# Kernel tuning notes

Measured on AMD Instinct MI355X. Metric: run time of the kernel, lower is better.

Reference implementation:

```python
import jax, jax.numpy as jnp
import numpy as np

NUM_HEADS = 4
NUM_GROUPS = 32
EPS = 1e-6


def group_norm(x, gamma, beta):
    # x: [b, c, h, w]
    b, c, h, w = x.shape
    xg = x.reshape(b, NUM_GROUPS, c // NUM_GROUPS, h, w)
    mu = xg.mean(axis=(2, 3, 4), keepdims=True)
    var = xg.var(axis=(2, 3, 4), keepdims=True)
    xn = ((xg - mu) * jax.lax.rsqrt(var + EPS)).reshape(b, c, h, w)
    return xn * gamma[None, :, None, None] + beta[None, :, None, None]


def conv1x1(x, W, b):
    # 1x1 conv == per-pixel channel matmul. W: [out_c, in_c], b: [out_c]
    return jnp.einsum('bchw,oc->bohw', x, W) + b[None, :, None, None]


def setup_inputs() -> dict:
    key = jax.random.key(0)
    ks = jax.random.split(key, 8)
    c = 256
    b, h, w = 1, 64, 64
    s = 1.0 / np.sqrt(c)
    return {
        'x_kv': jax.random.normal(ks[0], (b, c, h, w), dtype=jnp.float32),
        'gn_gamma': jnp.ones((c,), dtype=jnp.float32),
        'gn_beta': jnp.zeros((c,), dtype=jnp.float32),
        'Wq': jax.random.normal(ks[1], (c, c), dtype=jnp.float32) * s,
        'bq': jnp.zeros((c,), dtype=jnp.float32),
        'Wk': jax.random.normal(ks[2], (c, c), dtype=jnp.float32) * s,
        'bk': jnp.zeros((c,), dtype=jnp.float32),
        'Wv': jax.random.normal(ks[3], (c, c), dtype=jnp.float32) * s,
        'bv': jnp.zeros((c,), dtype=jnp.float32),
        'Wp': jax.random.normal(ks[4], (c, c), dtype=jnp.float32) * s,
        'bp': jnp.zeros((c,), dtype=jnp.float32),
    }


def reference(x_kv, gn_gamma, gn_beta, Wq, bq, Wk, bk, Wv, bv, Wp, bp):
    b, c, h, w = x_kv.shape
    hd = c // NUM_HEADS
    n = h * w

    h_norm = group_norm(x_kv, gn_gamma, gn_beta)  # self-attn: same norm for q,k,v

    q = conv1x1(h_norm, Wq, bq).reshape(b, NUM_HEADS, hd, n).transpose(0, 1, 3, 2)  # [b,H,n,hd]
    k = conv1x1(h_norm, Wk, bk).reshape(b, NUM_HEADS, hd, n)                        # [b,H,hd,n]
    v = conv1x1(h_norm, Wv, bv).reshape(b, NUM_HEADS, hd, n).transpose(0, 1, 3, 2)  # [b,H,n,hd]

    scores = jnp.einsum('bhnd,bhdm->bhnm', q, k) * (hd ** -0.5)  # [b,H,n,n]
    attn = jax.nn.softmax(scores, axis=-1)
    out = jnp.einsum('bhnm,bhmd->bhnd', attn, v)  # [b,H,n,hd]

    # Faithful to torch: permute(0,2,1,3).contiguous().view(b,c,h,w)
    out = out.transpose(0, 2, 1, 3).reshape(b, c, h, w)
    return x_kv + conv1x1(out, Wp, bp)
```

## Files before the change

### kernel.cpp

```cpp
#include <hip/hip_runtime.h>
#include <hip/hip_bf16.h>

#define NPIX 4096
#define CCH  256
#define HD   64
#define GSIZE 32768

typedef __bf16 bf16x8 __attribute__((ext_vector_type(8)));
typedef __bf16 bf16x4 __attribute__((ext_vector_type(4)));
typedef float  f32x4  __attribute__((ext_vector_type(4)));

#define XPITCH 264


__global__ __launch_bounds__(256) void stats_wconv(
    const float* __restrict__ X,
    const float* __restrict__ Wq, const float* __restrict__ Wk,
    const float* __restrict__ Wv, const float* __restrict__ Wp,
    float* __restrict__ psum, float* __restrict__ pssq, __bf16* __restrict__ Wb)
{
    const int bid = blockIdx.x, t = threadIdx.x;
    if (bid < 256) {
        const float* base = X + bid * 4096;
        float sum = 0.f, ssq = 0.f;
        #pragma unroll
        for (int k = 0; k < 4; ++k) {
            float4 v = *(const float4*)(base + t * 4 + k * 1024);
            sum += v.x + v.y + v.z + v.w;
            ssq += v.x * v.x + v.y * v.y + v.z * v.z + v.w * v.w;
        }
        #pragma unroll
        for (int off = 1; off < 64; off <<= 1) {
            sum += __shfl_xor(sum, off);
            ssq += __shfl_xor(ssq, off);
        }
        __shared__ float red[2][4];
        const int wv = t >> 6;
        if ((t & 63) == 0) { red[0][wv] = sum; red[1][wv] = ssq; }
        __syncthreads();
        if (t == 0) {
            psum[bid] = red[0][0] + red[0][1] + red[0][2] + red[0][3];
            pssq[bid] = red[1][0] + red[1][1] + red[1][2] + red[1][3];
        }
    } else {
        const int j0 = (bid - 256) * 4096 + t * 16;
        const int m  = j0 >> 16;
        const float* W = (m == 0) ? Wq : (m == 1) ? Wk : (m == 2) ? Wv : Wp;
        const float sc = (m == 0) ? 0.125f : 1.f;
        const int off = j0 & 65535;
        #pragma unroll
        for (int k = 0; k < 4; ++k) {
            float4 v = *(const float4*)(W + off + k * 4);
            bf16x4 o;
            o[0] = (__bf16)(v.x * sc); o[1] = (__bf16)(v.y * sc);
            o[2] = (__bf16)(v.z * sc); o[3] = (__bf16)(v.w * sc);
            *(bf16x4*)(Wb + m * 65536 + off + k * 4) = o;
        }
    }
}

__global__ __launch_bounds__(256) void gn_qkv(
    const float* __restrict__ X, const float* __restrict__ gamma,
    const float* __restrict__ beta,
    const float* __restrict__ psum, const float* __restrict__ pssq,
    const __bf16* __restrict__ Wb,
    const float* __restrict__ bq, const float* __restrict__ bk,
    const float* __restrict__ bv,
    __bf16* __restrict__ Qb, __bf16* __restrict__ Kb, __bf16* __restrict__ Vb)
{
    __shared__ __bf16 tile[64 * XPITCH];
    __shared__ float al[256], bl[256];

    const int t = threadIdx.x, lane = t & 63, wave = t >> 6;
    const int l16 = lane & 15, quad = lane >> 4;
    const int p0 = blockIdx.x * 64;
    const int z = blockIdx.y >> 1, och = blockIdx.y & 1;

    {
        const int g = t >> 3;
        float s = 0.f, q = 0.f;
        #pragma unroll
        for (int j = 0; j < 8; ++j) { s += psum[g * 8 + j]; q += pssq[g * 8 + j]; }
        const float mu  = s * (1.f / GSIZE);
        const float var = q * (1.f / GSIZE) - mu * mu;
        const float a = gamma[t] * rsqrtf(var + 1e-6f);
        al[t] = a;
        bl[t] = beta[t] - mu * a;
    }
    __syncthreads();

    #pragma unroll 4
    for (int i = 0; i < 16; ++i) {
        const int c4 = wave * 64 + i * 4;
        f32x4 a4 = *(const f32x4*)(al + c4);
        f32x4 b4 = *(const f32x4*)(bl + c4);
        bf16x4 pk;
        pk[0] = (__bf16)(X[(c4 + 0) * NPIX + p0 + lane] * a4[0] + b4[0]);
        pk[1] = (__bf16)(X[(c4 + 1) * NPIX + p0 + lane] * a4[1] + b4[1]);
        pk[2] = (__bf16)(X[(c4 + 2) * NPIX + p0 + lane] * a4[2] + b4[2]);
        pk[3] = (__bf16)(X[(c4 + 3) * NPIX + p0 + lane] * a4[3] + b4[3]);
        *(bf16x4*)(tile + lane * XPITCH + c4) = pk;
    }
    __syncthreads();

    const int pw = wave * 16;
    bf16x8 xf[8];
    #pragma unroll
    for (int kc = 0; kc < 8; ++kc)
        xf[kc] = *(const bf16x8*)(tile + (pw + l16) * XPITCH + kc * 32 + quad * 8);

    const __bf16* Wz = Wb + z * 65536;
    const float* bias = (z == 0) ? bq : (z == 1) ? bk : bv;

    if (z < 2) {
        const float qs = (z == 0) ? 0.125f : 1.f;
        __bf16* dst = (z == 0) ? Qb : Kb;
        #pragma unroll
        for (int grp = 0; grp < 2; ++grp) {
            f32x4 acc[4] = {};
            #pragma unroll
            for (int kc = 0; kc < 8; ++kc) {
                #pragma unroll
                for (int u = 0; u < 4; ++u) {
                    bf16x8 wf = *(const bf16x8*)(Wz + (och * 128 + (grp * 4 + u) * 16 + l16) * CCH + kc * 32 + quad * 8);
                    acc[u] = __builtin_amdgcn_mfma_f32_16x16x32_bf16(wf, xf[kc], acc[u], 0, 0, 0);
                }
            }
            #pragma unroll
            for (int u = 0; u < 4; ++u) {
                const int ot = och * 8 + grp * 4 + u;
                f32x4 bz = *(const f32x4*)(bias + och * 128 + (grp * 4 + u) * 16 + quad * 4);
                bf16x4 o;
                o[0] = (__bf16)(acc[u][0] + bz[0] * qs);
                o[1] = (__bf16)(acc[u][1] + bz[1] * qs);
                o[2] = (__bf16)(acc[u][2] + bz[2] * qs);
                o[3] = (__bf16)(acc[u][3] + bz[3] * qs);
                const int head = ot >> 2, dloc = (ot & 3) * 16 + quad * 4;
                *(bf16x4*)(dst + head * (NPIX * HD) + (p0 + pw + l16) * HD + dloc) = o;
            }
        }
    } else {
        #pragma unroll
        for (int grp = 0; grp < 2; ++grp) {
            f32x4 acc[4] = {};
            #pragma unroll
            for (int kc = 0; kc < 8; ++kc) {
                #pragma unroll
                for (int u = 0; u < 4; ++u) {
                    bf16x8 wf = *(const bf16x8*)(Wz + (och * 128 + (grp * 4 + u) * 16 + l16) * CCH + kc * 32 + quad * 8);
                    acc[u] = __builtin_amdgcn_mfma_f32_16x16x32_bf16(xf[kc], wf, acc[u], 0, 0, 0);
                }
            }
            #pragma unroll
            for (int u = 0; u < 4; ++u) {
                const int oc = och * 128 + (grp * 4 + u) * 16 + l16;
                const float bz = bias[oc];
                bf16x4 o;
                o[0] = (__bf16)(acc[u][0] + bz); o[1] = (__bf16)(acc[u][1] + bz);
                o[2] = (__bf16)(acc[u][2] + bz); o[3] = (__bf16)(acc[u][3] + bz);
                *(bf16x4*)(Vb + oc * NPIX + p0 + pw + quad * 4) = o;
            }
        }
    }
}

#define KPITCH 72
#define VPITCH 136
#define PPIT   40
#define KBUF   (128 * KPITCH)
#define VBUF   (64 * VPITCH)
#define OFF_K  0
#define OFF_V  (2 * KBUF * 2)
#define OFF_P  (OFF_V + 2 * VBUF * 2)
#define SMEMSZ (OFF_P + 4 * 64 * PPIT * 2)

__global__ __launch_bounds__(256, 1) void attn_mfma(
    const __bf16* __restrict__ Qb, const __bf16* __restrict__ Kb,
    const __bf16* __restrict__ Vb, __bf16* __restrict__ Sb)
{
    __shared__ __align__(16) char smem[SMEMSZ];
    __bf16* ktls = (__bf16*)(smem + OFF_K);
    __bf16* vtls = (__bf16*)(smem + OFF_V);
    __bf16* ptls = (__bf16*)(smem + OFF_P);
    float*  co   = (float*)smem;
    float*  cl   = (float*)(smem + 69632);

    const int t = threadIdx.x, lane = t & 63, wave = t >> 6;
    const int l16 = lane & 15, quad = lane >> 4;

    const int bid  = blockIdx.x;
    const int head = (bid & 7) >> 1;
    const int qt   = ((bid >> 3) << 1) | (bid & 1);
    const int p0   = qt * 64;

    const __bf16* Qh = Qb + head * (NPIX * HD);
    const __bf16* Kh = Kb + head * (NPIX * HD);
    const __bf16* Vh = Vb + head * (HD * NPIX);

    bf16x8 qf[4][2];
    #pragma unroll
    for (int rt = 0; rt < 4; ++rt) {
        const __bf16* qp = Qh + (p0 + rt * 16 + l16) * HD + quad * 8;
        qf[rt][0] = *(const bf16x8*)(qp);
        qf[rt][1] = *(const bf16x8*)(qp + 32);
    }

    bf16x8 ones;
    #pragma unroll
    for (int j = 0; j < 8; ++j) ones[j] = (__bf16)1.0f;

    f32x4 l_acc[4] = {};
    f32x4 o_acc[4][4] = {};

    __bf16* ptw = ptls + wave * (64 * PPIT);

    bf16x8 kpre[4], vpre[4];
    #pragma unroll
    for (int i = 0; i < 4; ++i) {
        const int c = t + 256 * i;
        kpre[i] = *(const bf16x8*)(Kh + (c >> 3) * HD + (c & 7) * 8);
        vpre[i] = *(const bf16x8*)(Vh + (c >> 4) * NPIX + (c & 15) * 8);
    }

    for (int it = 0; it < 32; ++it) {
        const int b = it & 1;
        __bf16* ktb = ktls + b * KBUF;
        __bf16* vtb = vtls + b * VBUF;

        #pragma unroll
        for (int i = 0; i < 4; ++i) {
            const int c = t + 256 * i;
            *(bf16x8*)(ktb + (c >> 3) * KPITCH + (c & 7) * 8)  = kpre[i];
            *(bf16x8*)(vtb + (c >> 4) * VPITCH + (c & 15) * 8) = vpre[i];
        }
        __syncthreads();

        if (it < 31) {
            const int kb = (it + 1) * 128;
            #pragma unroll
            for (int i = 0; i < 4; ++i) {
                const int c = t + 256 * i;
                kpre[i] = *(const bf16x8*)(Kh + (kb + (c >> 3)) * HD + (c & 7) * 8);
                vpre[i] = *(const bf16x8*)(Vh + (c >> 4) * NPIX + kb + (c & 15) * 8);
            }
        }

        bf16x8 kf[2][2], vf[4];
        #pragma unroll
        for (int kt = 0; kt < 2; ++kt) {
            const __bf16* kp = ktb + (wave * 32 + kt * 16 + l16) * KPITCH + quad * 8;
            kf[kt][0] = *(const bf16x8*)(kp);
            kf[kt][1] = *(const bf16x8*)(kp + 32);
        }
        #pragma unroll
        for (int dt = 0; dt < 4; ++dt)
            vf[dt] = *(const bf16x8*)(vtb + (dt * 16 + l16) * VPITCH + wave * 32 + quad * 8);

        f32x4 st[2][4] = {};
        #pragma unroll
        for (int kt = 0; kt < 2; ++kt)
            #pragma unroll
            for (int rt = 0; rt < 4; ++rt) {
                st[kt][rt] = __builtin_amdgcn_mfma_f32_16x16x32_bf16(kf[kt][0], qf[rt][0], st[kt][rt], 0, 0, 0);
                st[kt][rt] = __builtin_amdgcn_mfma_f32_16x16x32_bf16(kf[kt][1], qf[rt][1], st[kt][rt], 0, 0, 0);
            }

        #pragma unroll
        for (int kt = 0; kt < 2; ++kt)
            #pragma unroll
            for (int rt = 0; rt < 4; ++rt) {
                bf16x4 p;
                p[0] = (__bf16)__expf(st[kt][rt][0]);
                p[1] = (__bf16)__expf(st[kt][rt][1]);
                p[2] = (__bf16)__expf(st[kt][rt][2]);
                p[3] = (__bf16)__expf(st[kt][rt][3]);
                *(bf16x4*)(ptw + (rt * 16 + l16) * PPIT + kt * 16 + quad * 4) = p;
            }

        bf16x8 bp[4];
        #pragma unroll
        for (int rt = 0; rt < 4; ++rt)
            bp[rt] = *(const bf16x8*)(ptw + (rt * 16 + l16) * PPIT + quad * 8);

        #pragma unroll
        for (int rt = 0; rt < 4; ++rt)
            l_acc[rt] = __builtin_amdgcn_mfma_f32_16x16x32_bf16(ones, bp[rt], l_acc[rt], 0, 0, 0);

        #pragma unroll
        for (int dt = 0; dt < 4; ++dt)
            #pragma unroll
            for (int rt = 0; rt < 4; ++rt)
                o_acc[dt][rt] = __builtin_amdgcn_mfma_f32_16x16x32_bf16(vf[dt], bp[rt], o_acc[dt][rt], 0, 0, 0);
    }

    __syncthreads();

    #pragma unroll
    for (int dt = 0; dt < 4; ++dt)
        #pragma unroll
        for (int rt = 0; rt < 4; ++rt)
            *(f32x4*)(co + wave * 4352 + (rt * 16 + l16) * 68 + dt * 16 + quad * 4) = o_acc[dt][rt];
    if (quad == 0) {
        #pragma unroll
        for (int rt = 0; rt < 4; ++rt)
            cl[wave * 64 + rt * 16 + l16] = l_acc[rt][0];
    }
    __syncthreads();

    {
        const int row = t >> 2, dc = (t & 3) * 16;
        const float l = cl[row] + cl[64 + row] + cl[128 + row] + cl[192 + row];
        const float inv = 1.f / l;
        f32x4 s[4];
        #pragma unroll
        for (int j = 0; j < 4; ++j) {
            s[j] = f32x4{0.f, 0.f, 0.f, 0.f};
            #pragma unroll
            for (int w = 0; w < 4; ++w)
                s[j] += *(const f32x4*)(co + w * 4352 + row * 68 + dc + j * 4);
        }
        bf16x8 o1, o2;
        #pragma unroll
        for (int j = 0; j < 4; ++j) {
            o1[j]     = (__bf16)(s[0][j] * inv);
            o1[j + 4] = (__bf16)(s[1][j] * inv);
            o2[j]     = (__bf16)(s[2][j] * inv);
            o2[j + 4] = (__bf16)(s[3][j] * inv);
        }
        __bf16* dst = Sb + (p0 + row) * CCH + head * HD + dc;
        *(bf16x8*)(dst)     = o1;
        *(bf16x8*)(dst + 8) = o2;
    }
}

__global__ __launch_bounds__(256) void gemm_proj(
    const __bf16* __restrict__ Sb, const __bf16* __restrict__ Wpb,
    const float* __restrict__ bias, const float* __restrict__ X,
    float* __restrict__ Out)
{
    __shared__ __bf16 Bs[32 * XPITCH];

    const int t = threadIdx.x, lane = t & 63, wave = t >> 6;
    const int l16 = lane & 15, quad = lane >> 4;
    const int p0  = blockIdx.x * 32;
    const int och = blockIdx.y;

    #pragma unroll
    for (int pg = 0; pg < 4; ++pg) {
        bf16x8 v = *(const bf16x8*)(Sb + t * NPIX + p0 + pg * 8);
        #pragma unroll
        for (int j = 0; j < 8; ++j)
            Bs[(pg * 8 + j) * XPITCH + t] = v[j];
    }
    __syncthreads();

    const int pixset = wave & 1, ocset = wave >> 1;
    bf16x8 af[8];
    #pragma unroll
    for (int kc = 0; kc < 8; ++kc)
        af[kc] = *(const bf16x8*)(Bs + (pixset * 16 + l16) * XPITCH + kc * 32 + quad * 8);

    #pragma unroll
    for (int u = 0; u < 4; ++u) {
        f32x4 acc = {};
        const int oc_t = och * 128 + ocset * 64 + u * 16;
        #pragma unroll
        for (int kc = 0; kc < 8; ++kc) {
            bf16x8 wf = *(const bf16x8*)(Wpb + (oc_t + l16) * CCH + kc * 32 + quad * 8);
            acc = __builtin_amdgcn_mfma_f32_16x16x32_bf16(af[kc], wf, acc, 0, 0, 0);
        }
        const int oc  = oc_t + l16;
        const int pix = p0 + pixset * 16 + quad * 4;
        const float bz = bias[oc];
        f32x4 r4 = *(const f32x4*)(X + oc * NPIX + pix);
        f32x4 y;
        y[0] = acc[0] + bz + r4[0];
        y[1] = acc[1] + bz + r4[1];
        y[2] = acc[2] + bz + r4[2];
        y[3] = acc[3] + bz + r4[3];
        *(f32x4*)(Out + oc * NPIX + pix) = y;
    }
}

extern "C" void kernel_launch(void* const* d_in, const int* in_sizes, int n_in,
                              void* d_out, int out_size, void* d_ws, size_t ws_size,
                              hipStream_t stream)
{
    const float* x     = (const float*)d_in[0];
    const float* gamma = (const float*)d_in[1];
    const float* beta  = (const float*)d_in[2];
    const float* Wq    = (const float*)d_in[3];
    const float* bq    = (const float*)d_in[4];
    const float* Wk    = (const float*)d_in[5];
    const float* bk    = (const float*)d_in[6];
    const float* Wv    = (const float*)d_in[7];
    const float* bv    = (const float*)d_in[8];
    const float* Wp    = (const float*)d_in[9];
    const float* bp    = (const float*)d_in[10];
    float* out = (float*)d_out;

    char* ws = (char*)d_ws;
    float*  psum = (float*)(ws);
    float*  pssq = (float*)(ws + 1024);
    __bf16* Wb   = (__bf16*)(ws + 65536);
    __bf16* Qb   = (__bf16*)(ws + (1 << 20));
    __bf16* Kb   = (__bf16*)(ws + (3 << 20));
    __bf16* Vb   = (__bf16*)(ws + (5 << 20));
    __bf16* Sb   = (__bf16*)(ws + (7 << 20));

    stats_wconv<<<320, 256, 0, stream>>>(x, Wq, Wk, Wv, Wp, psum, pssq, Wb);

    dim3 gq(64, 6);
    gn_qkv<<<gq, 256, 0, stream>>>(x, gamma, beta, psum, pssq, Wb,
                                   bq, bk, bv, Qb, Kb, Vb);

    attn_mfma<<<256, 256, 0, stream>>>(Qb, Kb, Vb, Sb);

    dim3 gp(128, 2);
    gemm_proj<<<gp, 256, 0, stream>>>(Sb, Wb + 3 * 65536, bp, x, out);
}
```

Baseline: 151.6 us.

## Halve attention query tile to 32 rows and double grid for occupancy

The attention kernel now processes 32 query rows per block instead of 64 and launches 512 blocks rather than 256. Launch bounds move to two blocks per CU, and LDS pitches and the shared-memory layout shrink to fit. The aim is to fill more CUs and raise occupancy, hiding latency better. In exchange each K/V tile loaded from global memory is reused across fewer query rows, so K/V traffic doubles. The new K/V pitches (68/132) may also change LDS bank-conflict behaviour.

```diff
diff --git a/kernel.cpp b/kernel.cpp
--- a/kernel.cpp
+++ b/kernel.cpp
@@ -164,26 +164,25 @@
     }
 }
 
-#define KPITCH 72
-#define VPITCH 136
+#define KPITCH 68
+#define VPITCH 132
 #define PPIT   40
 #define KBUF   (128 * KPITCH)
 #define VBUF   (64 * VPITCH)
-#define OFF_K  0
 #define OFF_V  (2 * KBUF * 2)
 #define OFF_P  (OFF_V + 2 * VBUF * 2)
-#define SMEMSZ (OFF_P + 4 * 64 * PPIT * 2)
-
-__global__ __launch_bounds__(256, 1) void attn_mfma(
+#define SMEMSZ (OFF_P + 4 * 32 * PPIT * 2)
+
+__global__ __launch_bounds__(256, 2) void attn_mfma(
     const __bf16* __restrict__ Qb, const __bf16* __restrict__ Kb,
     const __bf16* __restrict__ Vb, __bf16* __restrict__ Sb)
 {
     __shared__ __align__(16) char smem[SMEMSZ];
-    __bf16* ktls = (__bf16*)(smem + OFF_K);
+    __bf16* ktls = (__bf16*)smem;
     __bf16* vtls = (__bf16*)(smem + OFF_V);
     __bf16* ptls = (__bf16*)(smem + OFF_P);
     float*  co   = (float*)smem;
-    float*  cl   = (float*)(smem + 69632);
+    float*  cl   = (float*)(smem + OFF_V);
 
     const int t = threadIdx.x, lane = t & 63, wave = t >> 6;
     const int l16 = lane & 15, quad = lane >> 4;
@@ -191,15 +190,15 @@
     const int bid  = blockIdx.x;
     const int head = (bid & 7) >> 1;
     const int qt   = ((bid >> 3) << 1) | (bid & 1);
-    const int p0   = qt * 64;
+    const int p0   = qt * 32;
 
     const __bf16* Qh = Qb + head * (NPIX * HD);
     const __bf16* Kh = Kb + head * (NPIX * HD);
     const __bf16* Vh = Vb + head * (HD * NPIX);
 
-    bf16x8 qf[4][2];
-    #pragma unroll
-    for (int rt = 0; rt < 4; ++rt) {
+    bf16x8 qf[2][2];
+    #pragma unroll
+    for (int rt = 0; rt < 2; ++rt) {
         const __bf16* qp = Qh + (p0 + rt * 16 + l16) * HD + quad * 8;
         qf[rt][0] = *(const bf16x8*)(qp);
         qf[rt][1] = *(const bf16x8*)(qp + 32);
@@ -209,10 +208,10 @@
     #pragma unroll
     for (int j = 0; j < 8; ++j) ones[j] = (__bf16)1.0f;
 
-    f32x4 l_acc[4] = {};
-    f32x4 o_acc[4][4] = {};
-
-    __bf16* ptw = ptls + wave * (64 * PPIT);
+    f32x4 l_acc[2] = {};
+    f32x4 o_acc[4][2] = {};
+
+    __bf16* ptw = ptls + wave * (32 * PPIT);
 
     bf16x8 kpre[4], vpre[4];
     #pragma unroll
@@ -256,11 +255,11 @@
         for (int dt = 0; dt < 4; ++dt)
             vf[dt] = *(const bf16x8*)(vtb + (dt * 16 + l16) * VPITCH + wave * 32 + quad * 8);
 
-        f32x4 st[2][4] = {};
+        f32x4 st[2][2] = {};
         #pragma unroll
         for (int kt = 0; kt < 2; ++kt)
             #pragma unroll
-            for (int rt = 0; rt < 4; ++rt) {
+            for (int rt = 0; rt < 2; ++rt) {
                 st[kt][rt] = __builtin_amdgcn_mfma_f32_16x16x32_bf16(kf[kt][0], qf[rt][0], st[kt][rt], 0, 0, 0);
                 st[kt][rt] = __builtin_amdgcn_mfma_f32_16x16x32_bf16(kf[kt][1], qf[rt][1], st[kt][rt], 0, 0, 0);
             }
@@ -268,7 +267,7 @@
         #pragma unroll
         for (int kt = 0; kt < 2; ++kt)
             #pragma unroll
-            for (int rt = 0; rt < 4; ++rt) {
+            for (int rt = 0; rt < 2; ++rt) {
                 bf16x4 p;
                 p[0] = (__bf16)__expf(st[kt][rt][0]);
                 p[1] = (__bf16)__expf(st[kt][rt][1]);
@@ -277,19 +276,19 @@
                 *(bf16x4*)(ptw + (rt * 16 + l16) * PPIT + kt * 16 + quad * 4) = p;
             }
 
-        bf16x8 bp[4];
-        #pragma unroll
-        for (int rt = 0; rt < 4; ++rt)
+        bf16x8 bp[2];
+        #pragma unroll
+        for (int rt = 0; rt < 2; ++rt)
             bp[rt] = *(const bf16x8*)(ptw + (rt * 16 + l16) * PPIT + quad * 8);
 
         #pragma unroll
-        for (int rt = 0; rt < 4; ++rt)
+        for (int rt = 0; rt < 2; ++rt)
             l_acc[rt] = __builtin_amdgcn_mfma_f32_16x16x32_bf16(ones, bp[rt], l_acc[rt], 0, 0, 0);
 
         #pragma unroll
         for (int dt = 0; dt < 4; ++dt)
             #pragma unroll
-            for (int rt = 0; rt < 4; ++rt)
+            for (int rt = 0; rt < 2; ++rt)
                 o_acc[dt][rt] = __builtin_amdgcn_mfma_f32_16x16x32_bf16(vf[dt], bp[rt], o_acc[dt][rt], 0, 0, 0);
     }
 
@@ -298,38 +297,31 @@
     #pragma unroll
     for (int dt = 0; dt < 4; ++dt)
         #pragma unroll
-        for (int rt = 0; rt < 4; ++rt)
-            *(f32x4*)(co + wave * 4352 + (rt * 16 + l16) * 68 + dt * 16 + quad * 4) = o_acc[dt][rt];
+        for (int rt = 0; rt < 2; ++rt)
+            *(f32x4*)(co + wave * 2176 + (rt * 16 + l16) * 68 + dt * 16 + quad * 4) = o_acc[dt][rt];
     if (quad == 0) {
         #pragma unroll
-        for (int rt = 0; rt < 4; ++rt)
-            cl[wave * 64 + rt * 16 + l16] = l_acc[rt][0];
+        for (int rt = 0; rt < 2; ++rt)
+            cl[wave * 32 + rt * 16 + l16] = l_acc[rt][0];
     }
     __syncthreads();
 
     {
-        const int row = t >> 2, dc = (t & 3) * 16;
-        const float l = cl[row] + cl[64 + row] + cl[128 + row] + cl[192 + row];
+        const int row = t >> 3, dg = (t & 7) * 8;
+        const float l = cl[row] + cl[32 + row] + cl[64 + row] + cl[96 + row];
         const float inv = 1.f / l;
-        f32x4 s[4];
-        #pragma unroll
-        for (int j = 0; j < 4; ++j) {
-            s[j] = f32x4{0.f, 0.f, 0.f, 0.f};
-            #pragma unroll
-            for (int w = 0; w < 4; ++w)
-                s[j] += *(const f32x4*)(co + w * 4352 + row * 68 + dc + j * 4);
-        }
-        bf16x8 o1, o2;
-        #pragma unroll
-        for (int j = 0; j < 4; ++j) {
-            o1[j]     = (__bf16)(s[0][j] * inv);
-            o1[j + 4] = (__bf16)(s[1][j] * inv);
-            o2[j]     = (__bf16)(s[2][j] * inv);
-            o2[j + 4] = (__bf16)(s[3][j] * inv);
-        }
-        __bf16* dst = Sb + (p0 + row) * CCH + head * HD + dc;
-        *(bf16x8*)(dst)     = o1;
-        *(bf16x8*)(dst + 8) = o2;
+        f32x4 s0 = {}, s1 = {};
+        #pragma unroll
+        for (int w = 0; w < 4; ++w) {
+            s0 += *(const f32x4*)(co + w * 2176 + row * 68 + dg);
+            s1 += *(const f32x4*)(co + w * 2176 + row * 68 + dg + 4);
+        }
+        bf16x8 o;
+        o[0] = (__bf16)(s0[0] * inv); o[1] = (__bf16)(s0[1] * inv);
+        o[2] = (__bf16)(s0[2] * inv); o[3] = (__bf16)(s0[3] * inv);
+        o[4] = (__bf16)(s1[0] * inv); o[5] = (__bf16)(s1[1] * inv);
+        o[6] = (__bf16)(s1[2] * inv); o[7] = (__bf16)(s1[3] * inv);
+        *(bf16x8*)(Sb + (p0 + row) * CCH + head * HD + dg) = o;
     }
 }
 
@@ -414,7 +406,7 @@
     gn_qkv<<<gq, 256, 0, stream>>>(x, gamma, beta, psum, pssq, Wb,
                                    bq, bk, bv, Qb, Kb, Vb);
 
-    attn_mfma<<<256, 256, 0, stream>>>(Qb, Kb, Vb, Sb);
+    attn_mfma<<<512, 256, 0, stream>>>(Qb, Kb, Vb, Sb);
 
     dim3 gp(128, 2);
     gemm_proj<<<gp, 256, 0, stream>>>(Sb, Wb + 3 * 65536, bp, x, out);
```

New measurement: 205.4 us. 1.35x slower.

## Single-buffer K/V tiles in LDS to fit two attention blocks per CU

Applied to the files above, without the earlier changes.

The attention kernel drops double-buffered K/V LDS tiles in favour of one shared buffer, with tighter row pitches. Each iteration now reads its K/V fragments, hits a barrier, writes the next tile from registers and prefetches the one after, then hits a second barrier at loop end. The smaller LDS footprint and launch bounds of 2 are meant to allow two resident blocks per CU. The cost is an extra barrier per iteration, a tighter register budget that may cause spills, and possibly more LDS bank conflicts from the new pitches.

```diff
diff --git a/kernel.cpp b/kernel.cpp
--- a/kernel.cpp
+++ b/kernel.cpp
@@ -164,23 +164,20 @@
     }
 }
 
-#define KPITCH 72
-#define VPITCH 136
+#define KPITCH 68
+#define VPITCH 132
 #define PPIT   40
-#define KBUF   (128 * KPITCH)
-#define VBUF   (64 * VPITCH)
-#define OFF_K  0
-#define OFF_V  (2 * KBUF * 2)
-#define OFF_P  (OFF_V + 2 * VBUF * 2)
-#define SMEMSZ (OFF_P + 4 * 64 * PPIT * 2)
-
-__global__ __launch_bounds__(256, 1) void attn_mfma(
+#define OFF_V  17408
+#define OFF_P  (OFF_V + 16896)
+#define SMEMSZ 70656
+
+__global__ __launch_bounds__(256, 2) void attn_mfma(
     const __bf16* __restrict__ Qb, const __bf16* __restrict__ Kb,
     const __bf16* __restrict__ Vb, __bf16* __restrict__ Sb)
 {
     __shared__ __align__(16) char smem[SMEMSZ];
-    __bf16* ktls = (__bf16*)(smem + OFF_K);
-    __bf16* vtls = (__bf16*)(smem + OFF_V);
+    __bf16* ktb  = (__bf16*)smem;
+    __bf16* vtb  = (__bf16*)(smem + OFF_V);
     __bf16* ptls = (__bf16*)(smem + OFF_P);
     float*  co   = (float*)smem;
     float*  cl   = (float*)(smem + 69632);
@@ -221,30 +218,21 @@
         kpre[i] = *(const bf16x8*)(Kh + (c >> 3) * HD + (c & 7) * 8);
         vpre[i] = *(const bf16x8*)(Vh + (c >> 4) * NPIX + (c & 15) * 8);
     }
+    #pragma unroll
+    for (int i = 0; i < 4; ++i) {
+        const int c = t + 256 * i;
+        *(bf16x8*)(ktb + (c >> 3) * KPITCH + (c & 7) * 8)  = kpre[i];
+        *(bf16x8*)(vtb + (c >> 4) * VPITCH + (c & 15) * 8) = vpre[i];
+    }
+    #pragma unroll
+    for (int i = 0; i < 4; ++i) {
+        const int c = t + 256 * i;
+        kpre[i] = *(const bf16x8*)(Kh + (128 + (c >> 3)) * HD + (c & 7) * 8);
+        vpre[i] = *(const bf16x8*)(Vh + (c >> 4) * NPIX + 128 + (c & 15) * 8);
+    }
+    __syncthreads();
 
     for (int it = 0; it < 32; ++it) {
-        const int b = it & 1;
-        __bf16* ktb = ktls + b * KBUF;
-        __bf16* vtb = vtls + b * VBUF;
-
-        #pragma unroll
-        for (int i = 0; i < 4; ++i) {
-            const int c = t + 256 * i;
-            *(bf16x8*)(ktb + (c >> 3) * KPITCH + (c & 7) * 8)  = kpre[i];
-            *(bf16x8*)(vtb + (c >> 4) * VPITCH + (c & 15) * 8) = vpre[i];
-        }
-        __syncthreads();
-
-        if (it < 31) {
-            const int kb = (it + 1) * 128;
-            #pragma unroll
-            for (int i = 0; i < 4; ++i) {
-                const int c = t + 256 * i;
-                kpre[i] = *(const bf16x8*)(Kh + (kb + (c >> 3)) * HD + (c & 7) * 8);
-                vpre[i] = *(const bf16x8*)(Vh + (c >> 4) * NPIX + kb + (c & 15) * 8);
-            }
-        }
-
         bf16x8 kf[2][2], vf[4];
         #pragma unroll
         for (int kt = 0; kt < 2; ++kt) {
@@ -255,6 +243,26 @@
         #pragma unroll
         for (int dt = 0; dt < 4; ++dt)
             vf[dt] = *(const bf16x8*)(vtb + (dt * 16 + l16) * VPITCH + wave * 32 + quad * 8);
+
+        __syncthreads();
+
+        if (it < 31) {
+            #pragma unroll
+            for (int i = 0; i < 4; ++i) {
+                const int c = t + 256 * i;
+                *(bf16x8*)(ktb + (c >> 3) * KPITCH + (c & 7) * 8)  = kpre[i];
+                *(bf16x8*)(vtb + (c >> 4) * VPITCH + (c & 15) * 8) = vpre[i];
+            }
+            if (it < 30) {
+                const int kb = (it + 2) * 128;
+                #pragma unroll
+                for (int i = 0; i < 4; ++i) {
+                    const int c = t + 256 * i;
+                    kpre[i] = *(const bf16x8*)(Kh + (kb + (c >> 3)) * HD + (c & 7) * 8);
+                    vpre[i] = *(const bf16x8*)(Vh + (c >> 4) * NPIX + kb + (c & 15) * 8);
+                }
+            }
+        }
 
         f32x4 st[2][4] = {};
         #pragma unroll
@@ -291,9 +299,9 @@
             #pragma unroll
             for (int rt = 0; rt < 4; ++rt)
                 o_acc[dt][rt] = __builtin_amdgcn_mfma_f32_16x16x32_bf16(vf[dt], bp[rt], o_acc[dt][rt], 0, 0, 0);
-    }
-
-    __syncthreads();
+
+        __syncthreads();
+    }
 
     #pragma unroll
     for (int dt = 0; dt < 4; ++dt)
```

Result: slower. 172.9 us (+14.1%).

## Fuse all four kernels into one persistent kernel with grid barriers

Applied to the files above, without the earlier changes.

Replaces the four separate launches (stats/weight convert, GN+QKV, attention, projection) with one 256-block persistent kernel whose phases are separated by atomic-counter grid barriers, plus a memset to reset the counters. The goal is to remove per-launch overhead and inter-kernel gaps. In exchange it adds barrier spin latency, relies on all 256 blocks being co-resident, and the QKV phase now runs 384 work units over 256 blocks, so some blocks do two.

```diff
diff --git a/kernel.cpp b/kernel.cpp
--- a/kernel.cpp
+++ b/kernel.cpp
@@ -10,375 +10,377 @@
 typedef __bf16 bf16x4 __attribute__((ext_vector_type(4)));
 typedef float  f32x4  __attribute__((ext_vector_type(4)));
 
+
 #define XPITCH 264
-
-
-__global__ __launch_bounds__(256) void stats_wconv(
-    const float* __restrict__ X,
-    const float* __restrict__ Wq, const float* __restrict__ Wk,
-    const float* __restrict__ Wv, const float* __restrict__ Wp,
-    float* __restrict__ psum, float* __restrict__ pssq, __bf16* __restrict__ Wb)
-{
-    const int bid = blockIdx.x, t = threadIdx.x;
-    if (bid < 256) {
-        const float* base = X + bid * 4096;
-        float sum = 0.f, ssq = 0.f;
-        #pragma unroll
-        for (int k = 0; k < 4; ++k) {
-            float4 v = *(const float4*)(base + t * 4 + k * 1024);
-            sum += v.x + v.y + v.z + v.w;
-            ssq += v.x * v.x + v.y * v.y + v.z * v.z + v.w * v.w;
-        }
-        #pragma unroll
-        for (int off = 1; off < 64; off <<= 1) {
-            sum += __shfl_xor(sum, off);
-            ssq += __shfl_xor(ssq, off);
-        }
-        __shared__ float red[2][4];
-        const int wv = t >> 6;
-        if ((t & 63) == 0) { red[0][wv] = sum; red[1][wv] = ssq; }
-        __syncthreads();
-        if (t == 0) {
-            psum[bid] = red[0][0] + red[0][1] + red[0][2] + red[0][3];
-            pssq[bid] = red[1][0] + red[1][1] + red[1][2] + red[1][3];
-        }
-    } else {
-        const int j0 = (bid - 256) * 4096 + t * 16;
-        const int m  = j0 >> 16;
-        const float* W = (m == 0) ? Wq : (m == 1) ? Wk : (m == 2) ? Wv : Wp;
-        const float sc = (m == 0) ? 0.125f : 1.f;
-        const int off = j0 & 65535;
-        #pragma unroll
-        for (int k = 0; k < 4; ++k) {
-            float4 v = *(const float4*)(W + off + k * 4);
-            bf16x4 o;
-            o[0] = (__bf16)(v.x * sc); o[1] = (__bf16)(v.y * sc);
-            o[2] = (__bf16)(v.z * sc); o[3] = (__bf16)(v.w * sc);
-            *(bf16x4*)(Wb + m * 65536 + off + k * 4) = o;
-        }
-    }
-}
-
-__global__ __launch_bounds__(256) void gn_qkv(
-    const float* __restrict__ X, const float* __restrict__ gamma,
-    const float* __restrict__ beta,
-    const float* __restrict__ psum, const float* __restrict__ pssq,
-    const __bf16* __restrict__ Wb,
-    const float* __restrict__ bq, const float* __restrict__ bk,
-    const float* __restrict__ bv,
-    __bf16* __restrict__ Qb, __bf16* __restrict__ Kb, __bf16* __restrict__ Vb)
-{
-    __shared__ __bf16 tile[64 * XPITCH];
-    __shared__ float al[256], bl[256];
-
-    const int t = threadIdx.x, lane = t & 63, wave = t >> 6;
-    const int l16 = lane & 15, quad = lane >> 4;
-    const int p0 = blockIdx.x * 64;
-    const int z = blockIdx.y >> 1, och = blockIdx.y & 1;
-
-    {
-        const int g = t >> 3;
-        float s = 0.f, q = 0.f;
-        #pragma unroll
-        for (int j = 0; j < 8; ++j) { s += psum[g * 8 + j]; q += pssq[g * 8 + j]; }
-        const float mu  = s * (1.f / GSIZE);
-        const float var = q * (1.f / GSIZE) - mu * mu;
-        const float a = gamma[t] * rsqrtf(var + 1e-6f);
-        al[t] = a;
-        bl[t] = beta[t] - mu * a;
-    }
-    __syncthreads();
-
-    #pragma unroll 4
-    for (int i = 0; i < 16; ++i) {
-        const int c4 = wave * 64 + i * 4;
-        f32x4 a4 = *(const f32x4*)(al + c4);
-        f32x4 b4 = *(const f32x4*)(bl + c4);
-        bf16x4 pk;
-        pk[0] = (__bf16)(X[(c4 + 0) * NPIX + p0 + lane] * a4[0] + b4[0]);
-        pk[1] = (__bf16)(X[(c4 + 1) * NPIX + p0 + lane] * a4[1] + b4[1]);
-        pk[2] = (__bf16)(X[(c4 + 2) * NPIX + p0 + lane] * a4[2] + b4[2]);
-        pk[3] = (__bf16)(X[(c4 + 3) * NPIX + p0 + lane] * a4[3] + b4[3]);
-        *(bf16x4*)(tile + lane * XPITCH + c4) = pk;
-    }
-    __syncthreads();
-
-    const int pw = wave * 16;
-    bf16x8 xf[8];
-    #pragma unroll
-    for (int kc = 0; kc < 8; ++kc)
-        xf[kc] = *(const bf16x8*)(tile + (pw + l16) * XPITCH + kc * 32 + quad * 8);
-
-    const __bf16* Wz = Wb + z * 65536;
-    const float* bias = (z == 0) ? bq : (z == 1) ? bk : bv;
-
-    if (z < 2) {
-        const float qs = (z == 0) ? 0.125f : 1.f;
-        __bf16* dst = (z == 0) ? Qb : Kb;
-        #pragma unroll
-        for (int grp = 0; grp < 2; ++grp) {
-            f32x4 acc[4] = {};
-            #pragma unroll
-            for (int kc = 0; kc < 8; ++kc) {
-                #pragma unroll
-                for (int u = 0; u < 4; ++u) {
-                    bf16x8 wf = *(const bf16x8*)(Wz + (och * 128 + (grp * 4 + u) * 16 + l16) * CCH + kc * 32 + quad * 8);
-                    acc[u] = __builtin_amdgcn_mfma_f32_16x16x32_bf16(wf, xf[kc], acc[u], 0, 0, 0);
-                }
-            }
-            #pragma unroll
-            for (int u = 0; u < 4; ++u) {
-                const int ot = och * 8 + grp * 4 + u;
-                f32x4 bz = *(const f32x4*)(bias + och * 128 + (grp * 4 + u) * 16 + quad * 4);
-                bf16x4 o;
-                o[0] = (__bf16)(acc[u][0] + bz[0] * qs);
-                o[1] = (__bf16)(acc[u][1] + bz[1] * qs);
-                o[2] = (__bf16)(acc[u][2] + bz[2] * qs);
-                o[3] = (__bf16)(acc[u][3] + bz[3] * qs);
-                const int head = ot >> 2, dloc = (ot & 3) * 16 + quad * 4;
-                *(bf16x4*)(dst + head * (NPIX * HD) + (p0 + pw + l16) * HD + dloc) = o;
-            }
-        }
-    } else {
-        #pragma unroll
-        for (int grp = 0; grp < 2; ++grp) {
-            f32x4 acc[4] = {};
-            #pragma unroll
-            for (int kc = 0; kc < 8; ++kc) {
-                #pragma unroll
-                for (int u = 0; u < 4; ++u) {
-                    bf16x8 wf = *(const bf16x8*)(Wz + (och * 128 + (grp * 4 + u) * 16 + l16) * CCH + kc * 32 + quad * 8);
-                    acc[u] = __builtin_amdgcn_mfma_f32_16x16x32_bf16(xf[kc], wf, acc[u], 0, 0, 0);
-                }
-            }
-            #pragma unroll
-            for (int u = 0; u < 4; ++u) {
-                const int oc = och * 128 + (grp * 4 + u) * 16 + l16;
-                const float bz = bias[oc];
-                bf16x4 o;
-                o[0] = (__bf16)(acc[u][0] + bz); o[1] = (__bf16)(acc[u][1] + bz);
-                o[2] = (__bf16)(acc[u][2] + bz); o[3] = (__bf16)(acc[u][3] + bz);
-                *(bf16x4*)(Vb + oc * NPIX + p0 + pw + quad * 4) = o;
-            }
-        }
-    }
-}
 
 #define KPITCH 72
 #define VPITCH 136
 #define PPIT   40
 #define KBUF   (128 * KPITCH)
 #define VBUF   (64 * VPITCH)
-#define OFF_K  0
 #define OFF_V  (2 * KBUF * 2)
 #define OFF_P  (OFF_V + 2 * VBUF * 2)
 #define SMEMSZ (OFF_P + 4 * 64 * PPIT * 2)
 
-__global__ __launch_bounds__(256, 1) void attn_mfma(
-    const __bf16* __restrict__ Qb, const __bf16* __restrict__ Kb,
-    const __bf16* __restrict__ Vb, __bf16* __restrict__ Sb)
+__device__ __forceinline__ void grid_barrier(unsigned* cnt, unsigned target)
+{
+    __syncthreads();
+    if (threadIdx.x == 0) {
+        __threadfence();
+        __hip_atomic_fetch_add(cnt, 1u, __ATOMIC_ACQ_REL, __HIP_MEMORY_SCOPE_AGENT);
+        while (__hip_atomic_load(cnt, __ATOMIC_ACQUIRE, __HIP_MEMORY_SCOPE_AGENT) < target)
+            __builtin_amdgcn_s_sleep(2);
+        __threadfence();
+    }
+    __syncthreads();
+}
+
+__global__ __launch_bounds__(256, 1) void fused_all(
+    const float* __restrict__ X, const float* __restrict__ gamma,
+    const float* __restrict__ beta,
+    const float* __restrict__ Wq, const float* __restrict__ bq,
+    const float* __restrict__ Wk, const float* __restrict__ bk,
+    const float* __restrict__ Wv, const float* __restrict__ bv,
+    const float* __restrict__ Wp, const float* __restrict__ bp,
+    float* __restrict__ Out,
+    float* __restrict__ psum, float* __restrict__ pssq, __bf16* __restrict__ Wb,
+    __bf16* __restrict__ Qb, __bf16* __restrict__ Kb, __bf16* __restrict__ Vb,
+    __bf16* __restrict__ Sb, unsigned* __restrict__ bar)
 {
     __shared__ __align__(16) char smem[SMEMSZ];
-    __bf16* ktls = (__bf16*)(smem + OFF_K);
-    __bf16* vtls = (__bf16*)(smem + OFF_V);
-    __bf16* ptls = (__bf16*)(smem + OFF_P);
-    float*  co   = (float*)smem;
-    float*  cl   = (float*)(smem + 69632);
 
     const int t = threadIdx.x, lane = t & 63, wave = t >> 6;
     const int l16 = lane & 15, quad = lane >> 4;
-
-    const int bid  = blockIdx.x;
-    const int head = (bid & 7) >> 1;
-    const int qt   = ((bid >> 3) << 1) | (bid & 1);
-    const int p0   = qt * 64;
-
-    const __bf16* Qh = Qb + head * (NPIX * HD);
-    const __bf16* Kh = Kb + head * (NPIX * HD);
-    const __bf16* Vh = Vb + head * (HD * NPIX);
-
-    bf16x8 qf[4][2];
-    #pragma unroll
-    for (int rt = 0; rt < 4; ++rt) {
-        const __bf16* qp = Qh + (p0 + rt * 16 + l16) * HD + quad * 8;
-        qf[rt][0] = *(const bf16x8*)(qp);
-        qf[rt][1] = *(const bf16x8*)(qp + 32);
+    const int bid = blockIdx.x;
+
+    {
+        const float* base = X + bid * 4096;
+        float sum = 0.f, ssq = 0.f;
+        #pragma unroll
+        for (int k = 0; k < 4; ++k) {
+            float4 v = *(const float4*)(base + t * 4 + k * 1024);
+            sum += v.x + v.y + v.z + v.w;
+            ssq += v.x * v.x + v.y * v.y + v.z * v.z + v.w * v.w;
+        }
+        #pragma unroll
+        for (int off = 1; off < 64; off <<= 1) {
+            sum += __shfl_xor(sum, off);
+            ssq += __shfl_xor(ssq, off);
+        }
+        float* red = (float*)smem;
+        if ((t & 63) == 0) { red[wave] = sum; red[4 + wave] = ssq; }
+        __syncthreads();
+        if (t == 0) {
+            psum[bid] = red[0] + red[1] + red[2] + red[3];
+            pssq[bid] = red[4] + red[5] + red[6] + red[7];
+        }
+        const int j0 = (bid * 256 + t) * 4;
+        const int m  = j0 >> 16;
+        const float* W = (m == 0) ? Wq : (m == 1) ? Wk : (m == 2) ? Wv : Wp;
+        const float sc = (m == 0) ? 0.125f : 1.f;
+        float4 v = *(const float4*)(W + (j0 & 65535));
+        bf16x4 o;
+        o[0] = (__bf16)(v.x * sc); o[1] = (__bf16)(v.y * sc);
+        o[2] = (__bf16)(v.z * sc); o[3] = (__bf16)(v.w * sc);
+        *(bf16x4*)(Wb + j0) = o;
     }
-
-    bf16x8 ones;
-    #pragma unroll
-    for (int j = 0; j < 8; ++j) ones[j] = (__bf16)1.0f;
-
-    f32x4 l_acc[4] = {};
-    f32x4 o_acc[4][4] = {};
-
-    __bf16* ptw = ptls + wave * (64 * PPIT);
-
-    bf16x8 kpre[4], vpre[4];
-    #pragma unroll
-    for (int i = 0; i < 4; ++i) {
-        const int c = t + 256 * i;
-        kpre[i] = *(const bf16x8*)(Kh + (c >> 3) * HD + (c & 7) * 8);
-        vpre[i] = *(const bf16x8*)(Vh + (c >> 4) * NPIX + (c & 15) * 8);
+    grid_barrier(bar + 0, 256);
+
+    {
+        __bf16* tile = (__bf16*)smem;
+        float*  al   = (float*)(smem + 33792);
+        float*  bl   = al + 256;
+
+        for (int u = bid; u < 384; u += 256) {
+            __syncthreads();
+            const int p0 = (u & 63) * 64;
+            const int zy = u >> 6;
+            const int z = zy >> 1, och = zy & 1;
+
+            {
+                const int g = t >> 3;
+                float s = 0.f, q = 0.f;
+                #pragma unroll
+                for (int j = 0; j < 8; ++j) { s += psum[g * 8 + j]; q += pssq[g * 8 + j]; }
+                const float mu  = s * (1.f / GSIZE);
+                const float var = q * (1.f / GSIZE) - mu * mu;
+                const float a = gamma[t] * rsqrtf(var + 1e-6f);
+                al[t] = a;
+                bl[t] = beta[t] - mu * a;
+            }
+            __syncthreads();
+
+            #pragma unroll 4
+            for (int i = 0; i < 16; ++i) {
+                const int c4 = wave * 64 + i * 4;
+                f32x4 a4 = *(const f32x4*)(al + c4);
+                f32x4 b4 = *(const f32x4*)(bl + c4);
+                bf16x4 pk;
+                pk[0] = (__bf16)(X[(c4 + 0) * NPIX + p0 + lane] * a4[0] + b4[0]);
+                pk[1] = (__bf16)(X[(c4 + 1) * NPIX + p0 + lane] * a4[1] + b4[1]);
+                pk[2] = (__bf16)(X[(c4 + 2) * NPIX + p0 + lane] * a4[2] + b4[2]);
+                pk[3] = (__bf16)(X[(c4 + 3) * NPIX + p0 + lane] * a4[3] + b4[3]);
+                *(bf16x4*)(tile + lane * XPITCH + c4) = pk;
+            }
+            __syncthreads();
+
+            const int pw = wave * 16;
+            bf16x8 xf[8];
+            #pragma unroll
+            for (int kc = 0; kc < 8; ++kc)
+                xf[kc] = *(const bf16x8*)(tile + (pw + l16) * XPITCH + kc * 32 + quad * 8);
+
+            const __bf16* Wz = Wb + z * 65536;
+            const float* bias = (z == 0) ? bq : (z == 1) ? bk : bv;
+
+            if (z < 2) {
+                const float qs = (z == 0) ? 0.125f : 1.f;
+                __bf16* dst = (z == 0) ? Qb : Kb;
+                #pragma unroll
+                for (int grp = 0; grp < 2; ++grp) {
+                    f32x4 acc[4] = {};
+                    #pragma unroll
+                    for (int kc = 0; kc < 8; ++kc) {
+                        #pragma unroll
+                        for (int uu = 0; uu < 4; ++uu) {
+                            bf16x8 wf = *(const bf16x8*)(Wz + (och * 128 + (grp * 4 + uu) * 16 + l16) * CCH + kc * 32 + quad * 8);
+                            acc[uu] = __builtin_amdgcn_mfma_f32_16x16x32_bf16(wf, xf[kc], acc[uu], 0, 0, 0);
+                        }
+                    }
+                    #pragma unroll
+                    for (int uu = 0; uu < 4; ++uu) {
+                        const int ot = och * 8 + grp * 4 + uu;
+                        f32x4 bz = *(const f32x4*)(bias + och * 128 + (grp * 4 + uu) * 16 + quad * 4);
+                        bf16x4 o;
+                        o[0] = (__bf16)(acc[uu][0] + bz[0] * qs);
+                        o[1] = (__bf16)(acc[uu][1] + bz[1] * qs);
+                        o[2] = (__bf16)(acc[uu][2] + bz[2] * qs);
+                        o[3] = (__bf16)(acc[uu][3] + bz[3] * qs);
+                        const int head = ot >> 2, dloc = (ot & 3) * 16 + quad * 4;
+                        *(bf16x4*)(dst + head * (NPIX * HD) + (p0 + pw + l16) * HD + dloc) = o;
+                    }
+                }
+            } else {
+                #pragma unroll
+                for (int grp = 0; grp < 2; ++grp) {
+                    f32x4 acc[4] = {};
+                    #pragma unroll
+                    for (int kc = 0; kc < 8; ++kc) {
+                        #pragma unroll
+                        for (int uu = 0; uu < 4; ++uu) {
+                            bf16x8 wf = *(const bf16x8*)(Wz + (och * 128 + (grp * 4 + uu) * 16 + l16) * CCH + kc * 32 + quad * 8);
+                            acc[uu] = __builtin_amdgcn_mfma_f32_16x16x32_bf16(xf[kc], wf, acc[uu], 0, 0, 0);
+                        }
+                    }
+                    #pragma unroll
+                    for (int uu = 0; uu < 4; ++uu) {
+                        const int oc = och * 128 + (grp * 4 + uu) * 16 + l16;
+                        const float bz = bias[oc];
+                        bf16x4 o;
+                        o[0] = (__bf16)(acc[uu][0] + bz); o[1] = (__bf16)(acc[uu][1] + bz);
+                        o[2] = (__bf16)(acc[uu][2] + bz); o[3] = (__bf16)(acc[uu][3] + bz);
+                        *(bf16x4*)(Vb + oc * NPIX + p0 + pw + quad * 4) = o;
+                    }
+                }
+            }
+        }
     }
-
-    for (int it = 0; it < 32; ++it) {
-        const int b = it & 1;
-        __bf16* ktb = ktls + b * KBUF;
-        __bf16* vtb = vtls + b * VBUF;
-
+    grid_barrier(bar + 1, 256);
+
+    {
+        __bf16* ktls = (__bf16*)smem;
+        __bf16* vtls = (__bf16*)(smem + OFF_V);
+        __bf16* ptls = (__bf16*)(smem + OFF_P);
+        float*  co   = (float*)smem;
+        float*  cl   = (float*)(smem + 69632);
+
+        const int head = (bid & 7) >> 1;
+        const int qt   = ((bid >> 3) << 1) | (bid & 1);
+        const int p0   = qt * 64;
+
+        const __bf16* Qh = Qb + head * (NPIX * HD);
+        const __bf16* Kh = Kb + head * (NPIX * HD);
+        const __bf16* Vh = Vb + head * (HD * NPIX);
+
+        bf16x8 qf[4][2];
+        #pragma unroll
+        for (int rt = 0; rt < 4; ++rt) {
+            const __bf16* qp = Qh + (p0 + rt * 16 + l16) * HD + quad * 8;
+            qf[rt][0] = *(const bf16x8*)(qp);
+            qf[rt][1] = *(const bf16x8*)(qp + 32);
+        }
+
+        bf16x8 ones;
+        #pragma unroll
+        for (int j = 0; j < 8; ++j) ones[j] = (__bf16)1.0f;
+
+        f32x4 l_acc[4] = {};
+        f32x4 o_acc[4][4] = {};
+
+        __bf16* ptw = ptls + wave * (64 * PPIT);
+
+        bf16x8 kpre[4], vpre[4];
         #pragma unroll
         for (int i = 0; i < 4; ++i) {
             const int c = t + 256 * i;
-            *(bf16x8*)(ktb + (c >> 3) * KPITCH + (c & 7) * 8)  = kpre[i];
-            *(bf16x8*)(vtb + (c >> 4) * VPITCH + (c & 15) * 8) = vpre[i];
-        }
-        __syncthreads();
-
-        if (it < 31) {
-            const int kb = (it + 1) * 128;
+            kpre[i] = *(const bf16x8*)(Kh + (c >> 3) * HD + (c & 7) * 8);
+            vpre[i] = *(const bf16x8*)(Vh + (c >> 4) * NPIX + (c & 15) * 8);
+        }
+
+        for (int it = 0; it < 32; ++it) {
+            const int b = it & 1;
+            __bf16* ktb = ktls + b * KBUF;
+            __bf16* vtb = vtls + b * VBUF;
+
             #pragma unroll
             for (int i = 0; i < 4; ++i) {
                 const int c = t + 256 * i;
-                kpre[i] = *(const bf16x8*)(Kh + (kb + (c >> 3)) * HD + (c & 7) * 8);
-                vpre[i] = *(const bf16x8*)(Vh + (c >> 4) * NPIX + kb + (c & 15) * 8);
-            }
-        }
-
-        bf16x8 kf[2][2], vf[4];
-        #pragma unroll
-        for (int kt = 0; kt < 2; ++kt) {
-            const __bf16* kp = ktb + (wave * 32 + kt * 16 + l16) * KPITCH + quad * 8;
-            kf[kt][0] = *(const bf16x8*)(kp);
-            kf[kt][1] = *(const bf16x8*)(kp + 32);
-        }
+                *(bf16x8*)(ktb + (c >> 3) * KPITCH + (c & 7) * 8)  = kpre[i];
+                *(bf16x8*)(vtb + (c >> 4) * VPITCH + (c & 15) * 8) = vpre[i];
+            }
+            __syncthreads();
+
+            if (it < 31) {
+                const int kb = (it + 1) * 128;
+                #pragma unroll
+                for (int i = 0; i < 4; ++i) {
+                    const int c = t + 256 * i;
+                    kpre[i] = *(const bf16x8*)(Kh + (kb + (c >> 3)) * HD + (c & 7) * 8);
+                    vpre[i] = *(const bf16x8*)(Vh + (c >> 4) * NPIX + kb + (c & 15) * 8);
+                }
+            }
+
+            bf16x8 kf[2][2], vf[4];
+            #pragma unroll
+            for (int kt = 0; kt < 2; ++kt) {
+                const __bf16* kp = ktb + (wave * 32 + kt * 16 + l16) * KPITCH + quad * 8;
+                kf[kt][0] = *(const bf16x8*)(kp);
+                kf[kt][1] = *(const bf16x8*)(kp + 32);
+            }
+            #pragma unroll
+            for (int dt = 0; dt < 4; ++dt)
+                vf[dt] = *(const bf16x8*)(vtb + (dt * 16 + l16) * VPITCH + wave * 32 + quad * 8);
+
+            f32x4 st[2][4] = {};
+            #pragma unroll
+            for (int kt = 0; kt < 2; ++kt)
+                #pragma unroll
+                for (int rt = 0; rt < 4; ++rt) {
+                    st[kt][rt] = __builtin_amdgcn_mfma_f32_16x16x32_bf16(kf[kt][0], qf[rt][0], st[kt][rt], 0, 0, 0);
+                    st[kt][rt] = __builtin_amdgcn_mfma_f32_16x16x32_bf16(kf[kt][1], qf[rt][1], st[kt][rt], 0, 0, 0);
+                }
+
+            #pragma unroll
+            for (int kt = 0; kt < 2; ++kt)
+                #pragma unroll
+                for (int rt = 0; rt < 4; ++rt) {
+                    bf16x4 p;
+                    p[0] = (__bf16)__expf(st[kt][rt][0]);
+                    p[1] = (__bf16)__expf(st[kt][rt][1]);
+                    p[2] = (__bf16)__expf(st[kt][rt][2]);
+                    p[3] = (__bf16)__expf(st[kt][rt][3]);
+                    *(bf16x4*)(ptw + (rt * 16 + l16) * PPIT + kt * 16 + quad * 4) = p;
+                }
+
+            bf16x8 bp2[4];
+            #pragma unroll
+            for (int rt = 0; rt < 4; ++rt)
+                bp2[rt] = *(const bf16x8*)(ptw + (rt * 16 + l16) * PPIT + quad * 8);
+
+            #pragma unroll
+            for (int rt = 0; rt < 4; ++rt)
+                l_acc[rt] = __builtin_amdgcn_mfma_f32_16x16x32_bf16(ones, bp2[rt], l_acc[rt], 0, 0, 0);
+
+            #pragma unroll
+            for (int dt = 0; dt < 4; ++dt)
+                #pragma unroll
+                for (int rt = 0; rt < 4; ++rt)
+                    o_acc[dt][rt] = __builtin_amdgcn_mfma_f32_16x16x32_bf16(vf[dt], bp2[rt], o_acc[dt][rt], 0, 0, 0);
+        }
+
+        __syncthreads();
+
         #pragma unroll
         for (int dt = 0; dt < 4; ++dt)
-            vf[dt] = *(const bf16x8*)(vtb + (dt * 16 + l16) * VPITCH + wave * 32 + quad * 8);
-
-        f32x4 st[2][4] = {};
-        #pragma unroll
-        for (int kt = 0; kt < 2; ++kt)
-            #pragma unroll
-            for (int rt = 0; rt < 4; ++rt) {
-                st[kt][rt] = __builtin_amdgcn_mfma_f32_16x16x32_bf16(kf[kt][0], qf[rt][0], st[kt][rt], 0, 0, 0);
-                st[kt][rt] = __builtin_amdgcn_mfma_f32_16x16x32_bf16(kf[kt][1], qf[rt][1], st[kt][rt], 0, 0, 0);
-            }
-
-        #pragma unroll
-        for (int kt = 0; kt < 2; ++kt)
-            #pragma unroll
-            for (int rt = 0; rt < 4; ++rt) {
-                bf16x4 p;
-                p[0] = (__bf16)__expf(st[kt][rt][0]);
-                p[1] = (__bf16)__expf(st[kt][rt][1]);
-                p[2] = (__bf16)__expf(st[kt][rt][2]);
-                p[3] = (__bf16)__expf(st[kt][rt][3]);
-                *(bf16x4*)(ptw + (rt * 16 + l16) * PPIT + kt * 16 + quad * 4) = p;
-            }
-
-        bf16x8 bp[4];
-        #pragma unroll
-        for (int rt = 0; rt < 4; ++rt)
-            bp[rt] = *(const bf16x8*)(ptw + (rt * 16 + l16) * PPIT + quad * 8);
-
-        #pragma unroll
-        for (int rt = 0; rt < 4; ++rt)
-            l_acc[rt] = __builtin_amdgcn_mfma_f32_16x16x32_bf16(ones, bp[rt], l_acc[rt], 0, 0, 0);
-
-        #pragma unroll
-        for (int dt = 0; dt < 4; ++dt)
             #pragma unroll
             for (int rt = 0; rt < 4; ++rt)
-                o_acc[dt][rt] = __builtin_amdgcn_mfma_f32_16x16x32_bf16(vf[dt], bp[rt], o_acc[dt][rt], 0, 0, 0);
+                *(f32x4*)(co + wave * 4352 + (rt * 16 + l16) * 68 + dt * 16 + quad * 4) = o_acc[dt][rt];
+        if (quad == 0) {
+            #pragma unroll
+            for (int rt = 0; rt < 4; ++rt)
+                cl[wave * 64 + rt * 16 + l16] = l_acc[rt][0];
+        }
+        __syncthreads();
+
+        {
+            const int row = t >> 2, dc = (t & 3) * 16;
+            const float l = cl[row] + cl[64 + row] + cl[128 + row] + cl[192 + row];
+            const float inv = 1.f / l;
+            f32x4 s[4];
+            #pragma unroll
+            for (int j = 0; j < 4; ++j) {
+                s[j] = f32x4{0.f, 0.f, 0.f, 0.f};
+                #pragma unroll
+                for (int w = 0; w < 4; ++w)
+                    s[j] += *(const f32x4*)(co + w * 4352 + row * 68 + dc + j * 4);
+            }
+            bf16x8 o1, o2;
+            #pragma unroll
+            for (int j = 0; j < 4; ++j) {
+                o1[j]     = (__bf16)(s[0][j] * inv);
+                o1[j + 4] = (__bf16)(s[1][j] * inv);
+                o2[j]     = (__bf16)(s[2][j] * inv);
+                o2[j + 4] = (__bf16)(s[3][j] * inv);
+            }
+            __bf16* dst = Sb + (p0 + row) * CCH + head * HD + dc;
+            *(bf16x8*)(dst)     = o1;
+            *(bf16x8*)(dst + 8) = o2;
+        }
     }
-
-    __syncthreads();
-
-    #pragma unroll
-    for (int dt = 0; dt < 4; ++dt)
-        #pragma unroll
-        for (int rt = 0; rt < 4; ++rt)
-            *(f32x4*)(co + wave * 4352 + (rt * 16 + l16) * 68 + dt * 16 + quad * 4) = o_acc[dt][rt];
-    if (quad == 0) {
-        #pragma unroll
-        for (int rt = 0; rt < 4; ++rt)
-            cl[wave * 64 + rt * 16 + l16] = l_acc[rt][0];
-    }
-    __syncthreads();
+    grid_barrier(bar + 2, 256);
 
     {
-        const int row = t >> 2, dc = (t & 3) * 16;
-        const float l = cl[row] + cl[64 + row] + cl[128 + row] + cl[192 + row];
-        const float inv = 1.f / l;
-        f32x4 s[4];
-        #pragma unroll
-        for (int j = 0; j < 4; ++j) {
-            s[j] = f32x4{0.f, 0.f, 0.f, 0.f};
-            #pragma unroll
-            for (int w = 0; w < 4; ++w)
-                s[j] += *(const f32x4*)(co + w * 4352 + row * 68 + dc + j * 4);
-        }
-        bf16x8 o1, o2;
-        #pragma unroll
-        for (int j = 0; j < 4; ++j) {
-            o1[j]     = (__bf16)(s[0][j] * inv);
-            o1[j + 4] = (__bf16)(s[1][j] * inv);
-            o2[j]     = (__bf16)(s[2][j] * inv);
-            o2[j + 4] = (__bf16)(s[3][j] * inv);
-        }
-        __bf16* dst = Sb + (p0 + row) * CCH + head * HD + dc;
-        *(bf16x8*)(dst)     = o1;
-        *(bf16x8*)(dst + 8) = o2;
-    }
-}
-
-__global__ __launch_bounds__(256) void gemm_proj(
-    const __bf16* __restrict__ Sb, const __bf16* __restrict__ Wpb,
-    const float* __restrict__ bias, const float* __restrict__ X,
-    float* __restrict__ Out)
-{
-    __shared__ __bf16 Bs[32 * XPITCH];
-
-    const int t = threadIdx.x, lane = t & 63, wave = t >> 6;
-    const int l16 = lane & 15, quad = lane >> 4;
-    const int p0  = blockIdx.x * 32;
-    const int och = blockIdx.y;
-
-    #pragma unroll
-    for (int pg = 0; pg < 4; ++pg) {
-        bf16x8 v = *(const bf16x8*)(Sb + t * NPIX + p0 + pg * 8);
-        #pragma unroll
-        for (int j = 0; j < 8; ++j)
-            Bs[(pg * 8 + j) * XPITCH + t] = v[j];
-    }
-    __syncthreads();
-
-    const int pixset = wave & 1, ocset = wave >> 1;
-    bf16x8 af[8];
-    #pragma unroll
-    for (int kc = 0; kc < 8; ++kc)
-        af[kc] = *(const bf16x8*)(Bs + (pixset * 16 + l16) * XPITCH + kc * 32 + quad * 8);
-
-    #pragma unroll
-    for (int u = 0; u < 4; ++u) {
-        f32x4 acc = {};
-        const int oc_t = och * 128 + ocset * 64 + u * 16;
-        #pragma unroll
-        for (int kc = 0; kc < 8; ++kc) {
-            bf16x8 wf = *(const bf16x8*)(Wpb + (oc_t + l16) * CCH + kc * 32 + quad * 8);
-            acc = __builtin_amdgcn_mfma_f32_16x16x32_bf16(af[kc], wf, acc, 0, 0, 0);
-        }
-        const int oc  = oc_t + l16;
-        const int pix = p0 + pixset * 16 + quad * 4;
-        const float bz = bias[oc];
-        f32x4 r4 = *(const f32x4*)(X + oc * NPIX + pix);
-        f32x4 y;
-        y[0] = acc[0] + bz + r4[0];
-        y[1] = acc[1] + bz + r4[1];
-        y[2] = acc[2] + bz + r4[2];
-        y[3] = acc[3] + bz + r4[3];
-        *(f32x4*)(Out + oc * NPIX + pix) = y;
+        __bf16* Bs = (__bf16*)smem;
+
+        const int p0  = (bid >> 1) * 32;
+        const int och = bid & 1;
+
+        #pragma unroll
+        for (int pg = 0; pg < 4; ++pg) {
+            bf16x8 v = *(const bf16x8*)(Sb + t * NPIX + p0 + pg * 8);
+            #pragma unroll
+            for (int j = 0; j < 8; ++j)
+                Bs[(pg * 8 + j) * XPITCH + t] = v[j];
+        }
+        __syncthreads();
+
+        const int pixset = wave & 1, ocset = wave >> 1;
+        bf16x8 af[8];
+        #pragma unroll
+        for (int kc = 0; kc < 8; ++kc)
+            af[kc] = *(const bf16x8*)(Bs + (pixset * 16 + l16) * XPITCH + kc * 32 + quad * 8);
+
+        const __bf16* Wpb = Wb + 3 * 65536;
+        #pragma unroll
+        for (int u = 0; u < 4; ++u) {
+            f32x4 acc = {};
+            const int oc_t = och * 128 + ocset * 64 + u * 16;
+            #pragma unroll
+            for (int kc = 0; kc < 8; ++kc) {
+                bf16x8 wf = *(const bf16x8*)(Wpb + (oc_t + l16) * CCH + kc * 32 + quad * 8);
+                acc = __builtin_amdgcn_mfma_f32_16x16x32_bf16(af[kc], wf, acc, 0, 0, 0);
+            }
+            const int oc  = oc_t + l16;
+            const int pix = p0 + pixset * 16 + quad * 4;
+            const float bz = bp[oc];
+            f32x4 r4 = *(const f32x4*)(X + oc * NPIX + pix);
+            f32x4 y;
+            y[0] = acc[0] + bz + r4[0];
+            y[1] = acc[1] + bz + r4[1];
+            y[2] = acc[2] + bz + r4[2];
+            y[3] = acc[3] + bz + r4[3];
+            *(f32x4*)(Out + oc * NPIX + pix) = y;
+        }
     }
 }
 
@@ -400,22 +402,19 @@
     float* out = (float*)d_out;
 
     char* ws = (char*)d_ws;
-    float*  psum = (float*)(ws);
-    float*  pssq = (float*)(ws + 1024);
-    __bf16* Wb   = (__bf16*)(ws + 65536);
-    __bf16* Qb   = (__bf16*)(ws + (1 << 20));
-    __bf16* Kb   = (__bf16*)(ws + (3 << 20));
-    __bf16* Vb   = (__bf16*)(ws + (5 << 20));
-    __bf16* Sb   = (__bf16*)(ws + (7 << 20));
-
-    stats_wconv<<<320, 256, 0, stream>>>(x, Wq, Wk, Wv, Wp, psum, pssq, Wb);
-
-    dim3 gq(64, 6);
-    gn_qkv<<<gq, 256, 0, stream>>>(x, gamma, beta, psum, pssq, Wb,
-                                   bq, bk, bv, Qb, Kb, Vb);
-
-    attn_mfma<<<256, 256, 0, stream>>>(Qb, Kb, Vb, Sb);
-
-    dim3 gp(128, 2);
-    gemm_proj<<<gp, 256, 0, stream>>>(Sb, Wb + 3 * 65536, bp, x, out);
+    float*    psum = (float*)(ws);
+    float*    pssq = (float*)(ws + 1024);
+    unsigned* bar  = (unsigned*)(ws + 4096);
+    __bf16*   Wb   = (__bf16*)(ws + 65536);
+    __bf16*   Qb   = (__bf16*)(ws + (1 << 20));
+    __bf16*   Kb   = (__bf16*)(ws + (3 << 20));
+    __bf16*   Vb   = (__bf16*)(ws + (5 << 20));
+    __bf16*   Sb   = (__bf16*)(ws + (7 << 20));
+
+    hipMemsetAsync(bar, 0, 64, stream);
+
+    fused_all<<<256, 256, 0, stream>>>(x, gamma, beta,
+                                       Wq, bq, Wk, bk, Wv, bv, Wp, bp,
+                                       out, psum, pssq, Wb,
+                                       Qb, Kb, Vb, Sb, bar);
 }
```

Measured after the change: 240.5 us. 58.7% more time.
